# Performance work log

Hardware: AMD Instinct MI355X
Metric: run time of the kernel (lower is better)

The kernel has to match this reference:

```python
import jax, jax.numpy as jnp
import numpy as np

B, N, C, DIN, DOUT = 16, 65536, 256, 16, 16  # ratio = N // C = 256 nodes per cluster


def setup_inputs() -> dict:
    key = jax.random.key(0)
    k1, k2, k3, k4, k5 = jax.random.split(key, 5)
    stdv = 1.0 / np.sqrt(DOUT)
    x = jax.random.normal(k1, (B, N, DIN), dtype=jnp.float32)
    # parameters, pre-reshaped: torch w_diag (in*out, C) with out-major io axis -> (out, in, C)
    w_diag = jax.random.uniform(k2, (DOUT, DIN, C), jnp.float32, -stdv, stdv)
    w_off = jax.random.uniform(k3, (DOUT, DIN, C, C), jnp.float32, -stdv, stdv)
    b1 = jax.random.uniform(k4, (DOUT,), jnp.float32, -stdv, stdv)
    # flatten_ids(cluster_ids): a permutation putting each cluster's nodes contiguous
    permute_ids = jax.random.permutation(k5, N)
    return {"x": x, "w_diag": w_diag, "w_off": w_off, "b1": b1, "permute_ids": permute_ids}


def reference(x, w_diag, w_off, b1, permute_ids):
    # Faithful to: W = rearrange(kron(diag_embed(w_diag), I_r)) + (1/N) rearrange(kron(w_off, 1_{rxr}))
    # out = inv_permute( reshape( W @ flatten(permute(x)) ) ) + b1,
    # computed via the block-constant structure instead of materializing the (Dout*N, Din*N) W.
    Bq, Nn, Din = x.shape
    Dout, _, Cc = w_diag.shape
    ratio = Nn // Cc
    inv_permute = jnp.argsort(permute_ids)
    xp = x[:, permute_ids, :]                       # (B, N, Din), cluster-contiguous
    xc = xp.reshape(Bq, Cc, ratio, Din)             # (B, C, r, Din)
    # diagonal blocks: per-cluster Din->Dout mixing, identity over within-cluster index
    out_diag = jnp.einsum('oic,bcri->bcro', w_diag, xc)   # (B, C, r, Dout)
    # off blocks: constant within each (cluster j, cluster k) block -> use cluster sums
    s = xc.sum(axis=2)                              # (B, C, Din)
    out_off = jnp.einsum('oick,bki->bco', w_off, s) / Nn  # (B, C, Dout)
    out = out_diag + out_off[:, :, None, :]         # broadcast over within-cluster index
    out = out.reshape(Bq, Nn, Dout)[:, inv_permute, :] + b1[None, None, :]
    return out
```

## Files before the change

### kernel.cpp

```cpp
#include <hip/hip_runtime.h>

#define B_    16
#define N_    65536
#define C_    256
#define DIN_  16
#define DOUT_ 16

typedef float f32x4 __attribute__((ext_vector_type(4)));


__global__ __launch_bounds__(256) void k_sum_prep(
    const float* __restrict__ x, const float* __restrict__ w_diag,
    const int* __restrict__ P, const float* __restrict__ b1,
    float* __restrict__ s, float* __restrict__ wd_t,
    int* __restrict__ c_of_n, float* __restrict__ off)
{
    int bid = blockIdx.x;
    int t = threadIdx.x;
    if (bid >= B_ * C_) {
        int r = bid - B_ * C_;
        if (r < 256) {
            int o = r >> 4, i = r & 15;
            wd_t[t * 256 + i * 16 + o] = w_diag[r * C_ + t];
        } else if (r < 512) {
            int k = r - 256;
            c_of_n[P[k * 256 + t]] = k;
        } else {
            int m = (r - 512) * 256 + t;
            off[m] = b1[m & 15];
        }
        return;
    }
    int b = bid >> 8;
    int k = bid & (C_ - 1);
    int q  = t & 3;
    int rg = t >> 2;
    float4 acc = make_float4(0.f, 0.f, 0.f, 0.f);
    const int jbase = k << 8;
    #pragma unroll
    for (int m = 0; m < 4; ++m) {
        int n = P[jbase + rg + 64 * m];
        const float4* row =
            reinterpret_cast<const float4*>(x + ((size_t)(b * N_ + n)) * DIN_);
        float4 v = row[q];
        acc.x += v.x; acc.y += v.y; acc.z += v.z; acc.w += v.w;
    }
    #pragma unroll
    for (int mask = 4; mask <= 32; mask <<= 1) {
        acc.x += __shfl_xor(acc.x, mask, 64);
        acc.y += __shfl_xor(acc.y, mask, 64);
        acc.z += __shfl_xor(acc.z, mask, 64);
        acc.w += __shfl_xor(acc.w, mask, 64);
    }
    __shared__ float4 part[4][4];
    int lane = t & 63, wave = t >> 6;
    if (lane < 4) part[wave][lane] = acc;
    __syncthreads();
    if (t < 16) {
        int qq = t >> 2, comp = t & 3;
        float v = 0.f;
        #pragma unroll
        for (int w = 0; w < 4; ++w) {
            const float* p = reinterpret_cast<const float*>(&part[w][qq]);
            v += p[comp];
        }
        int i = qq * 4 + comp;
        s[(b * DIN_ + i) * C_ + k] = v;
    }
}

__global__ __launch_bounds__(256) void k_off(
    const float* __restrict__ w_off, const float* __restrict__ s,
    float* __restrict__ off)
{
    const int g  = (int)blockIdx.x;
    const int c  = g & 255;
    const int r  = g >> 8;
    const int o0 = (r & 3) * 4;
    const int i0 = (r >> 2) * 8;
    const int t  = threadIdx.x;
    const int kq = t & 63;
    const int b0 = (t >> 6) * 4;

    const float4* w4 = reinterpret_cast<const float4*>(w_off);
    const float4* s4 = reinterpret_cast<const float4*>(s);

    const int wb = ((o0 * 16 + i0) * 256 + c) * 64 + kq;
    const int sb = (b0 * 16 + i0) * 64 + kq;

    float acc[16];
    #pragma unroll
    for (int z = 0; z < 16; ++z) acc[z] = 0.f;

    float4 wA0, wA1, wA2, wA3, sA0, sA1, sA2, sA3;
    float4 wB0, wB1, wB2, wB3, sB0, sB1, sB2, sB3;

#define LOADG(W0, W1, W2, W3, S0, S1, S2, S3, II)                              \
    W0 = w4[wb + 0 * 262144 + (II) * 16384];                                   \
    W1 = w4[wb + 1 * 262144 + (II) * 16384];                                   \
    W2 = w4[wb + 2 * 262144 + (II) * 16384];                                   \
    W3 = w4[wb + 3 * 262144 + (II) * 16384];                                   \
    S0 = s4[sb + 0 * 1024 + (II) * 64];                                        \
    S1 = s4[sb + 1 * 1024 + (II) * 64];                                        \
    S2 = s4[sb + 2 * 1024 + (II) * 64];                                        \
    S3 = s4[sb + 3 * 1024 + (II) * 64];

#define FMAG(W0, W1, W2, W3, S0, S1, S2, S3)                                   \
    {                                                                          \
        const float4 ww[4] = {W0, W1, W2, W3};                                 \
        const float4 ss[4] = {S0, S1, S2, S3};                                 \
        _Pragma("unroll")                                                      \
        for (int oo = 0; oo < 4; ++oo)                                         \
            _Pragma("unroll")                                                  \
            for (int bb = 0; bb < 4; ++bb)                                     \
                acc[oo * 4 + bb] += ww[oo].x * ss[bb].x + ww[oo].y * ss[bb].y  \
                                  + ww[oo].z * ss[bb].z + ww[oo].w * ss[bb].w; \
    }

    LOADG(wA0, wA1, wA2, wA3, sA0, sA1, sA2, sA3, 0)
    #pragma unroll
    for (int ii = 0; ii < 8; ii += 2) {
        LOADG(wB0, wB1, wB2, wB3, sB0, sB1, sB2, sB3, ii + 1)
        __builtin_amdgcn_sched_barrier(0);
        FMAG(wA0, wA1, wA2, wA3, sA0, sA1, sA2, sA3)
        if (ii + 2 < 8) {
            LOADG(wA0, wA1, wA2, wA3, sA0, sA1, sA2, sA3, ii + 2)
        }
        __builtin_amdgcn_sched_barrier(0);
        FMAG(wB0, wB1, wB2, wB3, sB0, sB1, sB2, sB3)
    }
#undef LOADG
#undef FMAG

#define FOLD(MASK, CNT)                                                        \
    {                                                                          \
        const bool hi_ = (kq & (MASK)) != 0;                                   \
        _Pragma("unroll")                                                      \
        for (int j = 0; j < (CNT); ++j) {                                      \
            float keep = hi_ ? acc[j + (CNT)] : acc[j];                        \
            float send = hi_ ? acc[j] : acc[j + (CNT)];                        \
            acc[j] = keep + __shfl_xor(send, (MASK), 64);                      \
        }                                                                      \
    }
    FOLD(1, 8) FOLD(2, 4) FOLD(4, 2) FOLD(8, 1)
#undef FOLD
    acc[0] += __shfl_xor(acc[0], 16, 64);
    acc[0] += __shfl_xor(acc[0], 32, 64);

    if (kq < 16) {
        int j  = ((kq & 1) << 3) | ((kq & 2) << 1) | ((kq & 4) >> 1) | ((kq & 8) >> 3);
        int oo = j >> 2;
        int bb = j & 3;
        int b  = b0 + bb;
        int o  = o0 + oo;
        atomicAdd(&off[((b << 8) + c) * DOUT_ + o], acc[0] * (1.0f / (float)N_));
    }
}

__global__ __launch_bounds__(256) void k_apply_seq(
    const float* __restrict__ x, const int* __restrict__ c_of_n,
    const float* __restrict__ wd_t, const float* __restrict__ off,
    float* __restrict__ out)
{
    int t = threadIdx.x;
    int lr = t >> 2, q = t & 3;
    int n = blockIdx.x * 64 + lr;
    int c = c_of_n[n];

    const float4* wd4 = reinterpret_cast<const float4*>(wd_t);
    float4 wds[16];
    #pragma unroll
    for (int i = 0; i < 16; ++i) wds[i] = wd4[c * 64 + i * 4 + q];

    const float4* x4   = reinterpret_cast<const float4*>(x);
    const float4* off4 = reinterpret_cast<const float4*>(off);
    f32x4* out4        = reinterpret_cast<f32x4*>(out);

    #pragma unroll 2
    for (int b = 0; b < B_; ++b) {
        size_t rowbase = ((size_t)(b * N_ + n)) * 4;
        float4 x0 = x4[rowbase + 0];
        float4 x1 = x4[rowbase + 1];
        float4 x2 = x4[rowbase + 2];
        float4 x3 = x4[rowbase + 3];
        float4 acc = off4[((size_t)((b << 8) + c)) * 4 + q];
        float xv[16];
        xv[0]=x0.x; xv[1]=x0.y; xv[2]=x0.z; xv[3]=x0.w;
        xv[4]=x1.x; xv[5]=x1.y; xv[6]=x1.z; xv[7]=x1.w;
        xv[8]=x2.x; xv[9]=x2.y; xv[10]=x2.z; xv[11]=x2.w;
        xv[12]=x3.x; xv[13]=x3.y; xv[14]=x3.z; xv[15]=x3.w;
        #pragma unroll
        for (int i = 0; i < 16; ++i) {
            acc.x += xv[i] * wds[i].x;
            acc.y += xv[i] * wds[i].y;
            acc.z += xv[i] * wds[i].z;
            acc.w += xv[i] * wds[i].w;
        }
        f32x4 accv;
        accv.x = acc.x; accv.y = acc.y; accv.z = acc.z; accv.w = acc.w;
        __builtin_nontemporal_store(accv, &out4[rowbase + q]);
    }
}

extern "C" void kernel_launch(void* const* d_in, const int* in_sizes, int n_in,
                              void* d_out, int out_size, void* d_ws, size_t ws_size,
                              hipStream_t stream) {
    const float* x      = (const float*)d_in[0];
    const float* w_diag = (const float*)d_in[1];
    const float* w_off  = (const float*)d_in[2];
    const float* b1     = (const float*)d_in[3];
    const int*   P      = (const int*)d_in[4];
    float* out    = (float*)d_out;
    float* s      = (float*)d_ws;
    float* off    = s + 65536;
    float* wd_t   = off + 65536;
    int*   c_of_n = (int*)(wd_t + 65536);

    k_sum_prep<<<B_ * C_ + 768, 256, 0, stream>>>(x, w_diag, P, b1,
                                                  s, wd_t, c_of_n, off);
    k_off<<<2048, 256, 0, stream>>>(w_off, s, off);
    k_apply_seq<<<N_ / 64, 256, 0, stream>>>(x, c_of_n, wd_t, off, out);
}
```

Baseline: 202.0 us.

## Retile k_off so each block covers 16 clusters for one output channel

Each k_off block now handles one output channel, half of the input channels and 16 consecutive clusters, with 64 accumulators per thread, instead of 4 output channels for a single cluster. The s loads are reused across 16 clusters rather than 4 output channels, and all 64 lanes end up holding a result after a full 6-level butterfly fold, so every lane issues an atomic. The grid drops from 2048 to 512 blocks. Register pressure rises sharply (64 accumulators plus 40 float4 buffers), which can reduce occupancy or cause spills.

```diff
diff --git a/kernel.cpp b/kernel.cpp
--- a/kernel.cpp
+++ b/kernel.cpp
@@ -73,61 +73,58 @@
     const float* __restrict__ w_off, const float* __restrict__ s,
     float* __restrict__ off)
 {
-    const int g  = (int)blockIdx.x;
-    const int c  = g & 255;
-    const int r  = g >> 8;
-    const int o0 = (r & 3) * 4;
-    const int i0 = (r >> 2) * 8;
-    const int t  = threadIdx.x;
-    const int kq = t & 63;
-    const int b0 = (t >> 6) * 4;
+    const int bid = (int)blockIdx.x;
+    const int cg  = bid & 15;
+    const int o   = (bid >> 4) & 15;
+    const int ih  = bid >> 8;
+    const int c0  = cg * 16;
+    const int t   = threadIdx.x;
+    const int kq  = t & 63;
+    const int b0  = (t >> 6) * 4;
 
     const float4* w4 = reinterpret_cast<const float4*>(w_off);
     const float4* s4 = reinterpret_cast<const float4*>(s);
 
-    const int wb = ((o0 * 16 + i0) * 256 + c) * 64 + kq;
-    const int sb = (b0 * 16 + i0) * 64 + kq;
-
-    float acc[16];
-    #pragma unroll
-    for (int z = 0; z < 16; ++z) acc[z] = 0.f;
-
-    float4 wA0, wA1, wA2, wA3, sA0, sA1, sA2, sA3;
-    float4 wB0, wB1, wB2, wB3, sB0, sB1, sB2, sB3;
-
-#define LOADG(W0, W1, W2, W3, S0, S1, S2, S3, II)                              \
-    W0 = w4[wb + 0 * 262144 + (II) * 16384];                                   \
-    W1 = w4[wb + 1 * 262144 + (II) * 16384];                                   \
-    W2 = w4[wb + 2 * 262144 + (II) * 16384];                                   \
-    W3 = w4[wb + 3 * 262144 + (II) * 16384];                                   \
-    S0 = s4[sb + 0 * 1024 + (II) * 64];                                        \
-    S1 = s4[sb + 1 * 1024 + (II) * 64];                                        \
-    S2 = s4[sb + 2 * 1024 + (II) * 64];                                        \
-    S3 = s4[sb + 3 * 1024 + (II) * 64];
-
-#define FMAG(W0, W1, W2, W3, S0, S1, S2, S3)                                   \
+    const int wbase = ((o * 16 + ih * 8) * 256 + c0) * 64 + kq;
+    const int sbase = (b0 * 16 + ih * 8) * 64 + kq;
+
+    float acc[64];
+    #pragma unroll
+    for (int z = 0; z < 64; ++z) acc[z] = 0.f;
+
+    float4 wA[16], sA[4], wB[16], sB[4];
+
+#define LOADG(WV, SV, II)                                                      \
     {                                                                          \
-        const float4 ww[4] = {W0, W1, W2, W3};                                 \
-        const float4 ss[4] = {S0, S1, S2, S3};                                 \
-        _Pragma("unroll")                                                      \
-        for (int oo = 0; oo < 4; ++oo)                                         \
+        _Pragma("unroll")                                                      \
+        for (int cc = 0; cc < 16; ++cc)                                        \
+            WV[cc] = w4[wbase + (II) * 16384 + cc * 64];                       \
+        _Pragma("unroll")                                                      \
+        for (int bb = 0; bb < 4; ++bb)                                         \
+            SV[bb] = s4[sbase + (II) * 64 + bb * 1024];                        \
+    }
+
+#define FMAG(WV, SV)                                                           \
+    {                                                                          \
+        _Pragma("unroll")                                                      \
+        for (int cc = 0; cc < 16; ++cc)                                        \
             _Pragma("unroll")                                                  \
             for (int bb = 0; bb < 4; ++bb)                                     \
-                acc[oo * 4 + bb] += ww[oo].x * ss[bb].x + ww[oo].y * ss[bb].y  \
-                                  + ww[oo].z * ss[bb].z + ww[oo].w * ss[bb].w; \
-    }
-
-    LOADG(wA0, wA1, wA2, wA3, sA0, sA1, sA2, sA3, 0)
+                acc[cc * 4 + bb] += WV[cc].x * SV[bb].x + WV[cc].y * SV[bb].y  \
+                                  + WV[cc].z * SV[bb].z + WV[cc].w * SV[bb].w; \
+    }
+
+    LOADG(wA, sA, 0)
     #pragma unroll
     for (int ii = 0; ii < 8; ii += 2) {
-        LOADG(wB0, wB1, wB2, wB3, sB0, sB1, sB2, sB3, ii + 1)
+        LOADG(wB, sB, ii + 1)
         __builtin_amdgcn_sched_barrier(0);
-        FMAG(wA0, wA1, wA2, wA3, sA0, sA1, sA2, sA3)
+        FMAG(wA, sA)
         if (ii + 2 < 8) {
-            LOADG(wA0, wA1, wA2, wA3, sA0, sA1, sA2, sA3, ii + 2)
+            LOADG(wA, sA, ii + 2)
         }
         __builtin_amdgcn_sched_barrier(0);
-        FMAG(wB0, wB1, wB2, wB3, sB0, sB1, sB2, sB3)
+        FMAG(wB, sB)
     }
 #undef LOADG
 #undef FMAG
@@ -142,19 +139,16 @@
             acc[j] = keep + __shfl_xor(send, (MASK), 64);                      \
         }                                                                      \
     }
-    FOLD(1, 8) FOLD(2, 4) FOLD(4, 2) FOLD(8, 1)
+    FOLD(1, 32) FOLD(2, 16) FOLD(4, 8) FOLD(8, 4) FOLD(16, 2) FOLD(32, 1)
 #undef FOLD
-    acc[0] += __shfl_xor(acc[0], 16, 64);
-    acc[0] += __shfl_xor(acc[0], 32, 64);
-
-    if (kq < 16) {
-        int j  = ((kq & 1) << 3) | ((kq & 2) << 1) | ((kq & 4) >> 1) | ((kq & 8) >> 3);
-        int oo = j >> 2;
-        int bb = j & 3;
-        int b  = b0 + bb;
-        int o  = o0 + oo;
-        atomicAdd(&off[((b << 8) + c) * DOUT_ + o], acc[0] * (1.0f / (float)N_));
-    }
+
+    int z = ((kq >> 5) & 1) | ((kq >> 3) & 2) | ((kq >> 1) & 4)
+          | ((kq << 1) & 8) | ((kq << 3) & 16) | ((kq << 5) & 32);
+    int cc = z >> 2;
+    int bb = z & 3;
+    int b  = b0 + bb;
+    int c  = c0 + cc;
+    atomicAdd(&off[((b << 8) + c) * DOUT_ + o], acc[0] * (1.0f / (float)N_));
 }
 
 __global__ __launch_bounds__(256) void k_apply_seq(
@@ -218,6 +212,6 @@
 
     k_sum_prep<<<B_ * C_ + 768, 256, 0, stream>>>(x, w_diag, P, b1,
                                                   s, wd_t, c_of_n, off);
-    k_off<<<2048, 256, 0, stream>>>(w_off, s, off);
+    k_off<<<512, 256, 0, stream>>>(w_off, s, off);
     k_apply_seq<<<N_ / 64, 256, 0, stream>>>(x, c_of_n, wd_t, off, out);
 }
```

Measured after the change: 342.9 us. 69.8% more time.
